# Optimization experiments

Hardware: AMD Instinct MI355X
Metric: run time of the kernel (lower is better)

Reference implementation:

```python
import jax, jax.numpy as jnp
import numpy as np

RNN_NUM = 4  # rnn_num mean-field iterations


def setup_inputs() -> dict:
    key = jax.random.key(0)
    k1, k2, k3, k4 = jax.random.split(key, 4)
    T, N, M, K = 16384, 256, 8, 16  # time steps, regions, features, gaussian kernels
    inputs = jax.random.normal(k1, (T, N, M), dtype=jnp.float32)
    kernels = jax.random.uniform(k2, (N, N, K), dtype=jnp.float32)  # positive -> stable denominator
    W_feat = jax.random.uniform(k3, (1, M), dtype=jnp.float32) * 0.01  # feature_linear_layer.weight (F_in[1]=1, F_in[0]=M)
    W_lin = jax.random.uniform(k4, (1, K), dtype=jnp.float32) * 0.01   # linear_layer.weight (1, D_in)
    return {"inputs": inputs, "kernels": kernels, "W_feat": W_feat, "W_lin": W_lin}


def reference(inputs, kernels, W_feat, W_lin):
    # inputs: (T, N, M); kernels: (N, N, K); W_feat: (1, M); W_lin: (1, K)
    x = inputs @ W_feat.T                 # feature_layer -> (T, N, 1)
    originals = x
    # feature_layer(ones(T,N,M)) is constant: every entry equals sum(W_feat)
    f_weights = jnp.sum(W_feat)           # scalar, broadcasts as (T, N, 1)
    # static_conv_layer(all_ones, kernels): conv1d with length-1 input of ones
    # == row-sum of each kernel slice -> (N, K); loop-invariant, compute once.
    ones_conv = kernels.sum(axis=1)       # (N, K)
    denom = f_weights + 2.0 * (ones_conv @ W_lin.T)  # (N, 1), broadcasts over T
    for _ in range(RNN_NUM):
        # static_conv_layer(x, kernels): conv1d(length=1) == matmul per kernel slice,
        # fused over all K slices: out[t,i,k] = sum_j x[t,j] * kernels[i,j,k]
        conv = jnp.einsum('tj,ijk->tik', x[:, :, 0], kernels)  # (T, N, K)
        numer = originals + 2.0 * (conv @ W_lin.T)             # (T, N, 1)
        x = numer / denom
    return x
```

## Files before the change

### kernel.cpp

```cpp
#include <hip/hip_runtime.h>


#define NREG 256
#define KG   16
#define MF   8

typedef unsigned short u16;
typedef __attribute__((ext_vector_type(8))) short short8;
typedef __attribute__((ext_vector_type(4))) float f32x4;

__device__ __forceinline__ void async_copy16(const void* g, void* l) {
    __builtin_amdgcn_global_load_lds(
        (const __attribute__((address_space(1))) void*)g,
        (__attribute__((address_space(3))) void*)l,
        16, 0, 0);
}

__device__ __forceinline__ f32x4 ld16(const float* p) {
    f32x4 d;
    asm volatile("global_load_dwordx4 %0, %1, off" : "=v"(d) : "v"(p));
    return d;
}

__device__ __forceinline__ u16 bf16_rne(float x) {
    unsigned u = __float_as_uint(x);
    return (u16)((u + 0x7FFFu + ((u >> 16) & 1u)) >> 16);
}
__device__ __forceinline__ float bf16_to_f(u16 h) {
    return __uint_as_float(((unsigned)h) << 16);
}

__global__ __launch_bounds__(256) void k_prep(const float* __restrict__ kern,
                                              const float* __restrict__ Wlin,
                                              const float* __restrict__ Wfeat,
                                              float* __restrict__ B,
                                              float* __restrict__ Einv) {
    const int i = blockIdx.x, j = threadIdx.x;
    const float* kp = kern + ((size_t)i * NREG + j) * KG;
    float4 w0 = *(const float4*)(Wlin + 0);
    float4 w1 = *(const float4*)(Wlin + 4);
    float4 w2 = *(const float4*)(Wlin + 8);
    float4 w3 = *(const float4*)(Wlin + 12);
    float4 v0 = *(const float4*)(kp + 0);
    float4 v1 = *(const float4*)(kp + 4);
    float4 v2 = *(const float4*)(kp + 8);
    float4 v3 = *(const float4*)(kp + 12);
    float km = v0.x*w0.x + v0.y*w0.y + v0.z*w0.z + v0.w*w0.w
             + v1.x*w1.x + v1.y*w1.y + v1.z*w1.z + v1.w*w1.w
             + v2.x*w2.x + v2.y*w2.y + v2.z*w2.z + v2.w*w2.w
             + v3.x*w3.x + v3.y*w3.y + v3.z*w3.z + v3.w*w3.w;

    __shared__ float red[256];
    red[j] = km;
    __syncthreads();
    for (int s = 128; s > 0; s >>= 1) {
        if (j < s) red[j] += red[j + s];
        __syncthreads();
    }
    __shared__ float sden;
    if (j == 0) {
        float fw = 0.f;
#pragma unroll
        for (int m = 0; m < MF; ++m) fw += Wfeat[m];
        float den = fw + 2.f * red[0];
        sden = den;
        Einv[i] = 1.f / den;
    }
    __syncthreads();
    B[(size_t)i * NREG + j] = 2.f * km / sden;
}

__global__ __launch_bounds__(512) void k_rows(const float* __restrict__ B,
                                              const float* __restrict__ Einv,
                                              u16* __restrict__ Mh,
                                              u16* __restrict__ Ml) {
    const int i = blockIdx.x;
    const int j = threadIdx.x & 255;
    const int h = threadIdx.x >> 8;
    const int l0 = h * 128;
    __shared__ float rB[NREG], rP[NREG];
    __shared__ float part[2][NREG];

    if (h == 0) rB[j] = B[(size_t)i * NREG + j];
    __syncthreads();

#define ROWMM(rowv, dst_write)                                                \
    {                                                                         \
        float acc = 0.f;                                                      \
        _Pragma("unroll 4")                                                   \
        for (int l = l0; l < l0 + 128; l += 8) {                              \
            float b0 = B[(size_t)(l + 0) * NREG + j];                         \
            float b1 = B[(size_t)(l + 1) * NREG + j];                         \
            float b2 = B[(size_t)(l + 2) * NREG + j];                         \
            float b3 = B[(size_t)(l + 3) * NREG + j];                         \
            float b4 = B[(size_t)(l + 4) * NREG + j];                         \
            float b5 = B[(size_t)(l + 5) * NREG + j];                         \
            float b6 = B[(size_t)(l + 6) * NREG + j];                         \
            float b7 = B[(size_t)(l + 7) * NREG + j];                         \
            acc += rowv[l+0]*b0 + rowv[l+1]*b1 + rowv[l+2]*b2 + rowv[l+3]*b3  \
                 + rowv[l+4]*b4 + rowv[l+5]*b5 + rowv[l+6]*b6 + rowv[l+7]*b7; \
        }                                                                     \
        part[h][j] = acc;                                                     \
        __syncthreads();                                                      \
        dst_write                                                             \
        __syncthreads();                                                      \
    }

    float b2v = 0.f, b3v = 0.f, b4v = 0.f;
    ROWMM(rB,  { b2v = part[0][j] + part[1][j]; if (h == 0) rP[j] = b2v; })
    ROWMM(rP,  { b3v = part[0][j] + part[1][j]; if (h == 1) rP[j] = b3v; })
    ROWMM(rP,  { b4v = part[0][j] + part[1][j]; })

    if (h == 0) {
        const size_t idx = (size_t)i * NREG + j;
        float v = ((i == j) ? 1.f : 0.f) + rB[j] + b2v + b3v;
        v = v * Einv[j] + b4v;
        u16 hh = bf16_rne(v);
        Mh[idx] = hh;
        Ml[idx] = bf16_rne(v - bf16_to_f(hh));
    }
}

__global__ __launch_bounds__(512, 1) void k_main(const float* __restrict__ in,
                                                 const float* __restrict__ Wfeat,
                                                 const u16* __restrict__ Mh,
                                                 const u16* __restrict__ Ml,
                                                 float* __restrict__ out) {
    __shared__ __align__(16) u16 Ah[64 * 256];
    __shared__ __align__(16) u16 Al[64 * 256];
    __shared__ __align__(16) u16 Bh[256 * 64];
    __shared__ __align__(16) u16 Bl[256 * 64];

    const int tid = threadIdx.x, lane = tid & 63, wid = tid >> 6;
    const size_t t0 = (size_t)blockIdx.x * 64;

    float4 wa = *(const float4*)(Wfeat);
    float4 wb = *(const float4*)(Wfeat + 4);
    asm volatile("" :: "v"(wa.x), "v"(wa.y), "v"(wa.z), "v"(wa.w),
                       "v"(wb.x), "v"(wb.y), "v"(wb.z), "v"(wb.w));

    const float* rowbase = in + (t0 + wid * 8) * (NREG * MF);

#define ISSUE(BUF, TL)                                                        \
    {                                                                         \
        const float* rp_ = rowbase + (TL) * 2048 + lane * 8;                  \
        _Pragma("unroll")                                                     \
        for (int q = 0; q < 8; ++q)                                           \
            BUF[q] = ld16(rp_ + (q >> 1) * 512 + (q & 1) * 4);                \
    }

#define PROCESS(BUF, TL)                                                      \
    {                                                                         \
        const int t_ = wid * 8 + (TL);                                        \
        _Pragma("unroll")                                                     \
        for (int dq = 0; dq < 4; ++dq) {                                      \
            f32x4 a0 = BUF[2 * dq], a1 = BUF[2 * dq + 1];                     \
            float o = a0[0]*wa.x + a0[1]*wa.y + a0[2]*wa.z + a0[3]*wa.w       \
                    + a1[0]*wb.x + a1[1]*wb.y + a1[2]*wb.z + a1[3]*wb.w;      \
            u16 h_ = bf16_rne(o);                                             \
            u16 l_ = bf16_rne(o - bf16_to_f(h_));                             \
            const int j_ = dq * 64 + lane;                                    \
            const int idx_ = t_ * 256 + (((j_ >> 3) ^ (TL)) * 8) + (j_ & 7);  \
            Ah[idx_] = h_;                                                    \
            Al[idx_] = l_;                                                    \
        }                                                                     \
    }

#define WAITV(N)  asm volatile("s_waitcnt vmcnt(" #N ")" ::: "memory");       \
                  __builtin_amdgcn_sched_barrier(0);

    f32x4 ba[8], bb[8], bc[8];
    ISSUE(ba, 0)
    ISSUE(bb, 1)
    ISSUE(bc, 2)
    WAITV(16)  PROCESS(ba, 0)  ISSUE(ba, 3)
    WAITV(16)  PROCESS(bb, 1)  ISSUE(bb, 4)
    WAITV(16)  PROCESS(bc, 2)  ISSUE(bc, 5)
    WAITV(16)  PROCESS(ba, 3)  ISSUE(ba, 6)
    WAITV(16)  PROCESS(bb, 4)  ISSUE(bb, 7)
    WAITV(16)  PROCESS(bc, 5)
    WAITV(8)   PROCESS(ba, 6)
    WAITV(0)   PROCESS(bb, 7)

    __syncthreads();

    const int mrow = (wid >> 1) * 16 + (lane & 15);
    const int nh   = (wid & 1) * 8;
    f32x4 acc[8];
#pragma unroll
    for (int n = 0; n < 8; ++n) acc[n] = (f32x4){0.f, 0.f, 0.f, 0.f};

    for (int p = 0; p < 4; ++p) {
        if (p) __syncthreads();
#pragma unroll
        for (int s = 0; s < 8; ++s) {
            const int g = s * 8 + wid;
            const int i0 = (g & 31) * 8;
            const u16* sg = (g >> 5) ? Ml : Mh;
            u16* dg = (g >> 5) ? Bl : Bh;
            const int irow = i0 + (lane >> 3);
            const int ch = (lane & 7) ^ (lane >> 3);
            async_copy16(sg + (size_t)irow * NREG + p * 64 + ch * 8,
                         dg + i0 * 64);
        }
        __syncthreads();

#pragma unroll
        for (int kst = 0; kst < 2; ++kst) {
            const int achunk = (8 * p + 4 * kst + (lane >> 4)) ^ (lane & 7);
            short8 a_h = *(const short8*)(Ah + mrow * 256 + achunk * 8);
            short8 a_l = *(const short8*)(Al + mrow * 256 + achunk * 8);
#pragma unroll
            for (int n = 0; n < 8; ++n) {
                const int irow = (nh + n) * 16 + (lane & 15);
                const int bchunk = (4 * kst + (lane >> 4)) ^ (lane & 7);
                short8 b_h = *(const short8*)(Bh + irow * 64 + bchunk * 8);
                short8 b_l = *(const short8*)(Bl + irow * 64 + bchunk * 8);
                acc[n] = __builtin_amdgcn_mfma_f32_16x16x32_bf16(a_h, b_h, acc[n], 0, 0, 0);
                acc[n] = __builtin_amdgcn_mfma_f32_16x16x32_bf16(a_h, b_l, acc[n], 0, 0, 0);
                acc[n] = __builtin_amdgcn_mfma_f32_16x16x32_bf16(a_l, b_h, acc[n], 0, 0, 0);
            }
        }
    }

    const size_t tbase = t0 + (wid >> 1) * 16 + (lane >> 4) * 4;
#pragma unroll
    for (int n = 0; n < 8; ++n) {
#pragma unroll
        for (int r = 0; r < 4; ++r) {
            out[(tbase + r) * NREG + (nh + n) * 16 + (lane & 15)] = acc[n][r];
        }
    }
}

extern "C" void kernel_launch(void* const* d_in, const int* in_sizes, int n_in,
                              void* d_out, int out_size, void* d_ws, size_t ws_size,
                              hipStream_t stream) {
    const float* inputs  = (const float*)d_in[0];
    const float* kernels = (const float*)d_in[1];
    const float* Wfeat   = (const float*)d_in[2];
    const float* Wlin    = (const float*)d_in[3];
    float* out = (float*)d_out;

    float* ws   = (float*)d_ws;
    float* B    = ws;
    float* Einv = B + NREG * NREG;
    u16*   Mh   = (u16*)(Einv + NREG);
    u16*   Ml   = Mh + NREG * NREG;

    k_prep <<<256, 256, 0, stream>>>(kernels, Wlin, Wfeat, B, Einv);
    k_rows <<<256, 512, 0, stream>>>(B, Einv, Mh, Ml);
    k_main <<<256, 512, 0, stream>>>(inputs, Wfeat, Mh, Ml, out);
}
```

Measured before the change: 49.19 us.

## Prefetch first B tile early and deepen input load pipeline to four buffers

The async copy of the first 64-column slice of the split-bf16 kernel matrix now starts before the input feature loads, so it overlaps with the streaming of inputs. The register-buffered input pipeline grows from three to four buffers, keeping more global loads in flight, and the vmcnt waits are adjusted to match. Later B slices are staged at the end of each iteration rather than at the start. This aims to hide memory latency in a bandwidth-bound kernel, at the cost of extra VGPRs for the fourth buffer.

```diff
diff --git a/kernel.cpp b/kernel.cpp
--- a/kernel.cpp
+++ b/kernel.cpp
@@ -139,6 +139,23 @@
     asm volatile("" :: "v"(wa.x), "v"(wa.y), "v"(wa.z), "v"(wa.w),
                        "v"(wb.x), "v"(wb.y), "v"(wb.z), "v"(wb.w));
 
+#define STAGEB(P)                                                             \
+    {                                                                         \
+        _Pragma("unroll")                                                     \
+        for (int s = 0; s < 8; ++s) {                                         \
+            const int g = s * 8 + wid;                             \
+            const int i0 = (g & 31) * 8;                                      \
+            const u16* sg = (g >> 5) ? Ml : Mh;                               \
+            u16* dg = (g >> 5) ? Bl : Bh;                                     \
+            const int irow = i0 + (lane >> 3);                                \
+            const int ch = (lane & 7) ^ (lane >> 3);                          \
+            async_copy16(sg + (size_t)irow * NREG + (P) * 64 + ch * 8,        \
+                         dg + i0 * 64);                                       \
+        }                                                                     \
+    }
+
+    STAGEB(0)
+
     const float* rowbase = in + (t0 + wid * 8) * (NREG * MF);
 
 #define ISSUE(BUF, TL)                                                        \
@@ -169,18 +186,19 @@
 #define WAITV(N)  asm volatile("s_waitcnt vmcnt(" #N ")" ::: "memory");       \
                   __builtin_amdgcn_sched_barrier(0);
 
-    f32x4 ba[8], bb[8], bc[8];
+    f32x4 ba[8], bb[8], bc[8], bd[8];
     ISSUE(ba, 0)
     ISSUE(bb, 1)
     ISSUE(bc, 2)
-    WAITV(16)  PROCESS(ba, 0)  ISSUE(ba, 3)
-    WAITV(16)  PROCESS(bb, 1)  ISSUE(bb, 4)
-    WAITV(16)  PROCESS(bc, 2)  ISSUE(bc, 5)
-    WAITV(16)  PROCESS(ba, 3)  ISSUE(ba, 6)
-    WAITV(16)  PROCESS(bb, 4)  ISSUE(bb, 7)
-    WAITV(16)  PROCESS(bc, 5)
-    WAITV(8)   PROCESS(ba, 6)
-    WAITV(0)   PROCESS(bb, 7)
+    ISSUE(bd, 3)
+    WAITV(24)  PROCESS(ba, 0)  ISSUE(ba, 4)
+    WAITV(24)  PROCESS(bb, 1)  ISSUE(bb, 5)
+    WAITV(24)  PROCESS(bc, 2)  ISSUE(bc, 6)
+    WAITV(24)  PROCESS(bd, 3)  ISSUE(bd, 7)
+    WAITV(24)  PROCESS(ba, 4)
+    WAITV(16)  PROCESS(bb, 5)
+    WAITV(8)   PROCESS(bc, 6)
+    WAITV(0)   PROCESS(bd, 7)
 
     __syncthreads();
 
@@ -191,20 +209,6 @@
     for (int n = 0; n < 8; ++n) acc[n] = (f32x4){0.f, 0.f, 0.f, 0.f};
 
     for (int p = 0; p < 4; ++p) {
-        if (p) __syncthreads();
-#pragma unroll
-        for (int s = 0; s < 8; ++s) {
-            const int g = s * 8 + wid;
-            const int i0 = (g & 31) * 8;
-            const u16* sg = (g >> 5) ? Ml : Mh;
-            u16* dg = (g >> 5) ? Bl : Bh;
-            const int irow = i0 + (lane >> 3);
-            const int ch = (lane & 7) ^ (lane >> 3);
-            async_copy16(sg + (size_t)irow * NREG + p * 64 + ch * 8,
-                         dg + i0 * 64);
-        }
-        __syncthreads();
-
 #pragma unroll
         for (int kst = 0; kst < 2; ++kst) {
             const int achunk = (8 * p + 4 * kst + (lane >> 4)) ^ (lane & 7);
@@ -221,6 +225,11 @@
                 acc[n] = __builtin_amdgcn_mfma_f32_16x16x32_bf16(a_l, b_h, acc[n], 0, 0, 0);
             }
         }
+        if (p < 3) {
+            __syncthreads();
+            STAGEB(p + 1)
+            __syncthreads();
+        }
     }
 
     const size_t tbase = t0 + (wid >> 1) * 16 + (lane >> 4) * 4;
```

Result: no change. 48.73 us (-0.9%).
